# Performance work log

Hardware: AMD Instinct MI355X
Metric: run time of the kernel (lower is better)

The kernel has to match this reference:

```python
import jax, jax.numpy as jnp
import numpy as np

B, L, S, H, E = 2, 2048, 2048, 16, 64


def setup_inputs() -> dict:
    key = jax.random.key(0)
    kq, kk, kv = jax.random.split(key, 3)
    queries = jax.random.normal(kq, (B, L, H, E), dtype=jnp.float32)
    keys = jax.random.normal(kk, (B, S, H, E), dtype=jnp.float32)
    values = jax.random.normal(kv, (B, S, H, E), dtype=jnp.float32)
    attn_mask = jnp.ones((B, 1, L, S), dtype=jnp.float32)  # >0.5 means attend
    return {"queries": queries, "keys": keys, "values": values, "attn_mask": attn_mask}


def reference(queries, keys, values, attn_mask):
    # queries: [B,L,H,E], keys/values: [B,S,H,E], attn_mask broadcastable to [B,H,L,S]
    E_ = queries.shape[-1]
    scale = 1.0 / np.sqrt(E_).astype(np.float32)
    scores = jnp.einsum('blhe,bshe->bhls', queries, keys)  # [B,H,L,S]
    large_negative = jnp.float32(-1e9)
    scores = scores + jnp.where(attn_mask > 0.5, jnp.float32(0.0), large_negative)
    A = jax.nn.softmax(scale * scores, axis=-1)  # dropout p=0.0 -> identity
    V = jnp.einsum('bhls,bshd->bhld', A, values)  # [B,H,L,D]
    return V
```

## Files before the change

### kernel.cpp

```cpp
#include <hip/hip_runtime.h>

typedef float    f32x4 __attribute__((ext_vector_type(4)));
typedef _Float16 f16x2 __attribute__((ext_vector_type(2)));
typedef _Float16 f16x4 __attribute__((ext_vector_type(4)));
typedef _Float16 f16x8 __attribute__((ext_vector_type(8)));
typedef int      i32x4 __attribute__((ext_vector_type(4)));

namespace {
constexpr int B_ = 2, L_ = 2048, S_ = 2048, H_ = 16, E_ = 64;
constexpr int MBLK = 128;
constexpr int NT = 64;
constexpr int NTILES = S_ / NT;

#define SCALE2f 0.1803368801111204f
#define MBIAS2f -1.8033688e8f

constexpr size_t KHOFF = (size_t)1 << 20;
constexpr size_t VHOFF = KHOFF + (size_t)B_ * H_ * S_ * E_ * 2;

__device__ __forceinline__ f16x2 cvt2(float a, float b) {
  return __builtin_bit_cast(f16x2, __builtin_amdgcn_cvt_pkrtz(a, b));
}
__device__ __forceinline__ int pkh(float a, float b) {
  return __builtin_bit_cast(int, __builtin_amdgcn_cvt_pkrtz(a, b));
}
union H8 { f16x8 v; i32x4 i; };
union H4 { f16x4 v; f16x2 h[2]; };

#define GLOAD_LDS16(g, l)                                              \
  __builtin_amdgcn_global_load_lds(                                    \
      (const __attribute__((address_space(1))) void*)(g),              \
      (__attribute__((address_space(3))) void*)(l), 16, 0, 0)
}

extern "C" __global__ __launch_bounds__(256)
void maskpack_kernel(const float* __restrict__ Mg, unsigned long long* __restrict__ Wb) {
  const int w    = (int)((blockIdx.x * 256 + threadIdx.x) >> 6);
  const int lane = threadIdx.x & 63;
  const float* src = Mg + (size_t)w * 2048 + lane;
  unsigned long long* dst = Wb + (size_t)w * 32;
#pragma unroll 8
  for (int j = 0; j < 32; ++j) {
    const unsigned long long bits = __ballot(src[j * 64] > 0.5f);
    if (lane == 0) dst[j] = bits;
  }
}

extern "C" __global__ __launch_bounds__(256)
void kcvt_kernel(const float* __restrict__ Kg, _Float16* __restrict__ Kh) {
  const int idx = blockIdx.x * 256 + threadIdx.x;
  const int j = idx & 7;
  const int h = (idx >> 3) & (H_ - 1);
  const int s = (idx >> 7) & (S_ - 1);
  const int b = idx >> 18;
  const float* src = Kg + ((((size_t)b * S_ + s) * H_ + h) << 6) + j * 8;
  f32x4 x = *(const f32x4*)src, y = *(const f32x4*)(src + 4);
  i32x4 w = {pkh(x[0], x[1]), pkh(x[2], x[3]), pkh(y[0], y[1]), pkh(y[2], y[3])};
  *(i32x4*)(Kh + ((((size_t)b * H_ + h) * S_ + s) << 6) + j * 8) = w;
}

extern "C" __global__ __launch_bounds__(256)
void vcvt_kernel(const float* __restrict__ Vg, _Float16* __restrict__ Vh) {
  __shared__ _Float16 T[64][72];
  const int bid = blockIdx.x;
  const int st = bid & 31;
  const int h  = (bid >> 5) & (H_ - 1);
  const int b  = bid >> 9;
  const int t  = threadIdx.x;
  const int sl = t >> 2;
  const int e0 = (t & 3) << 4;
  const float* src = Vg + ((((size_t)b * S_ + st * 64 + sl) * H_ + h) << 6) + e0;
#pragma unroll
  for (int i = 0; i < 4; ++i) {
    f32x4 x = *(const f32x4*)(src + i * 4);
#pragma unroll
    for (int c = 0; c < 4; ++c) T[e0 + i * 4 + c][sl] = (_Float16)x[c];
  }
  __syncthreads();
  const int er = t >> 2;
  const int s0 = (t & 3) << 4;
  _Float16* dst = Vh + (((((size_t)b * H_ + h) << 6) + er) * S_) + st * 64 + s0;
  *(i32x4*)dst       = *(const i32x4*)&T[er][s0];
  *(i32x4*)(dst + 8) = *(const i32x4*)&T[er][s0 + 8];
}

extern "C" __global__ __launch_bounds__(256, 2)
void fattn_kernel(const float* __restrict__ Qg, const _Float16* __restrict__ Kh,
                  const _Float16* __restrict__ Vh, const unsigned long long* __restrict__ Wb,
                  float* __restrict__ Og) {
  __shared__ __align__(16) _Float16 Ks[2][NT][64];
  __shared__ __align__(16) _Float16 Vt[2][E_][64];

  const int tid  = threadIdx.x;
  const int wv   = tid >> 6;
  const int lane = tid & 63;
  const int qd   = lane >> 4;
  const int cl   = lane & 15;
  const int sw   = cl & 7;

  const int bid = blockIdx.x;
  const int qb  = bid >> 5;
  const int bh  = bid & 31;
  const int h   = bh & (H_ - 1);
  const int b   = bh >> 4;

  const int l0 = qb * MBLK + wv * 32;

  f16x8 qf[2][2];
#pragma unroll
  for (int mt = 0; mt < 2; ++mt) {
    const float* qp = Qg + ((((size_t)b * L_ + (l0 + mt * 16 + cl)) * H_ + h) << 6);
#pragma unroll
    for (int kb = 0; kb < 2; ++kb) {
      const int e0 = qd * 8 + kb * 32;
      f32x4 x = *(const f32x4*)(qp + e0);
      f32x4 y = *(const f32x4*)(qp + e0 + 4);
      H8 u;
      u.i = (i32x4){pkh(x[0], x[1]), pkh(x[2], x[3]), pkh(y[0], y[1]), pkh(y[2], y[3])};
      qf[mt][kb] = u.v;
    }
  }

  const int rl  = lane >> 3;
  const int gsl = lane & 7;
  const int gsw = gsl ^ rl;
  const _Float16* khb = Kh + ((((size_t)b * H_ + h) * S_) << 6);
  const _Float16* vhb = Vh + ((((size_t)b * H_ + h) << 6) * (size_t)S_);

  const unsigned long long* wbp = Wb + (((size_t)b * L_ + (l0 + cl)) << 5);

  auto dma = [&](int buf, int t) {
#pragma unroll
    for (int p = 0; p < 2; ++p) {
      const int r0 = p * 32 + wv * 8;
      const _Float16* ksrc = khb + (((size_t)(t * 64 + r0 + rl)) << 6) + gsw * 8;
      GLOAD_LDS16(ksrc, &Ks[buf][r0][0]);
      const _Float16* vsrc = vhb + (size_t)(r0 + rl) * S_ + t * 64 + gsw * 8;
      GLOAD_LDS16(vsrc, &Vt[buf][r0][0]);
    }
  };

  const f32x4 zero4 = {0.f, 0.f, 0.f, 0.f};
  f32x4 acc[2][4];
#pragma unroll
  for (int mt = 0; mt < 2; ++mt)
#pragma unroll
    for (int et = 0; et < 4; ++et) acc[mt][et] = zero4;
  f32x4 rs4[2] = {zero4, zero4};

  dma(0, 0);
  unsigned long long mwcur = wbp[0];

  for (int t = 0; t < NTILES; ++t) {
    const int cb = t & 1;
    __syncthreads();

    if (t + 1 < NTILES) dma(cb ^ 1, t + 1);
    unsigned long long mwnext = 0;
    if (t + 1 < NTILES) mwnext = wbp[t + 1];

    f32x4 sc[4][2];
#pragma unroll
    for (int nt = 0; nt < 4; ++nt) {
      const _Float16* krow = &Ks[cb][nt * 16 + cl][0];
      const f16x8 a0 = *(const f16x8*)(krow + ((qd ^ sw) << 3));
      const f16x8 a1 = *(const f16x8*)(krow + (((qd + 4) ^ sw) << 3));
#pragma unroll
      for (int mt = 0; mt < 2; ++mt) {
        f32x4 c = zero4;
        c = __builtin_amdgcn_mfma_f32_16x16x32_f16(a0, qf[mt][0], c, 0, 0, 0);
        c = __builtin_amdgcn_mfma_f32_16x16x32_f16(a1, qf[mt][1], c, 0, 0, 0);
        sc[nt][mt] = c;
      }
    }

    f16x4 pa[2][4];
    if (mwcur == ~0ull) {
#pragma unroll
      for (int mt = 0; mt < 2; ++mt)
#pragma unroll
        for (int nt = 0; nt < 4; ++nt) {
          f32x4 p;
#pragma unroll
          for (int r = 0; r < 4; ++r)
            p[r] = __builtin_amdgcn_exp2f(sc[nt][mt][r] * SCALE2f);
          rs4[mt] += p;
          H4 u;
          u.h[0] = cvt2(p[0], p[1]);
          u.h[1] = cvt2(p[2], p[3]);
          pa[mt][nt] = u.v;
        }
    } else {
      const unsigned lo = (unsigned)mwcur;
      const unsigned hi = (unsigned)(mwcur >> 32);
#pragma unroll
      for (int mt = 0; mt < 2; ++mt)
#pragma unroll
        for (int nt = 0; nt < 4; ++nt) {
          const unsigned shm = ((nt < 2) ? lo : hi) >> ((nt & 1) * 16 + qd * 4);
          f32x4 p;
#pragma unroll
          for (int r = 0; r < 4; ++r) {
            const float bias = (shm & (1u << r)) ? 0.f : MBIAS2f;
            p[r] = __builtin_amdgcn_exp2f(__builtin_fmaf(sc[nt][mt][r], SCALE2f, bias));
          }
          rs4[mt] += p;
          H4 u;
          u.h[0] = cvt2(p[0], p[1]);
          u.h[1] = cvt2(p[2], p[3]);
          pa[mt][nt] = u.v;
        }
    }

#pragma unroll
    for (int nt = 0; nt < 4; ++nt)
#pragma unroll
      for (int et = 0; et < 4; ++et) {
        const _Float16* vrow = &Vt[cb][et * 16 + cl][0];
        const f16x4 bv = *(const f16x4*)(vrow + ((((2 * nt + (qd >> 1)) ^ sw) << 3) + ((qd & 1) << 2)));
        acc[0][et] = __builtin_amdgcn_mfma_f32_16x16x16f16(pa[0][nt], bv, acc[0][et], 0, 0, 0);
        acc[1][et] = __builtin_amdgcn_mfma_f32_16x16x16f16(pa[1][nt], bv, acc[1][et], 0, 0, 0);
      }

    mwcur = mwnext;
  }

#pragma unroll
  for (int mt = 0; mt < 2; ++mt) {
    float v = rs4[mt][0] + rs4[mt][1] + rs4[mt][2] + rs4[mt][3];
    v += __shfl_xor(v, 16, 64);
    v += __shfl_xor(v, 32, 64);
#pragma unroll
    for (int r = 0; r < 4; ++r) {
      const float invq = 1.0f / __shfl(v, qd * 4 + r, 64);
      const int l = l0 + mt * 16 + qd * 4 + r;
      float* op = Og + ((((size_t)b * H_ + h) * L_ + l) << 6) + cl;
#pragma unroll
      for (int et = 0; et < 4; ++et) op[et * 16] = acc[mt][et][r] * invq;
    }
  }
}

extern "C" void kernel_launch(void* const* d_in, const int* in_sizes, int n_in,
                              void* d_out, int out_size, void* d_ws, size_t ws_size,
                              hipStream_t stream) {
  const float* Q = (const float*)d_in[0];
  const float* K = (const float*)d_in[1];
  const float* V = (const float*)d_in[2];
  const float* M = (const float*)d_in[3];
  float* O = (float*)d_out;
  unsigned long long* Wb = (unsigned long long*)d_ws;
  _Float16* Khp = (_Float16*)((char*)d_ws + KHOFF);
  _Float16* Vhp = (_Float16*)((char*)d_ws + VHOFF);

  hipLaunchKernelGGL(maskpack_kernel, dim3(B_ * L_ / 4), dim3(256), 0, stream, M, Wb);
  hipLaunchKernelGGL(kcvt_kernel, dim3(B_ * S_ * H_ * 8 / 256), dim3(256), 0, stream, K, Khp);
  hipLaunchKernelGGL(vcvt_kernel, dim3(B_ * H_ * (S_ / 64)), dim3(256), 0, stream, V, Vhp);
  hipLaunchKernelGGL(fattn_kernel, dim3(B_ * H_ * (L_ / MBLK)), dim3(256), 0, stream,
                     Q, Khp, Vhp, Wb, O);
}
```

Measured before the change: 177.1 us.

## Use 8 waves of 16 query rows per block and vectorize mask packing

The attention kernel now runs 512 threads per block, with each wave owning 16 query rows instead of 32. Register pressure per wave drops and more waves are resident to hide latency, but each K/V tile in LDS is reused by fewer rows per wave. The mask packer now has each thread read 16 contiguous floats with vector loads and write a 16-bit word, replacing per-wave ballots with strided scalar loads.

New measurement: 166.6 us. -5.9%, faster.

```diff
diff --git a/kernel.cpp b/kernel.cpp
--- a/kernel.cpp
+++ b/kernel.cpp
@@ -35,15 +35,16 @@
 
 extern "C" __global__ __launch_bounds__(256)
 void maskpack_kernel(const float* __restrict__ Mg, unsigned long long* __restrict__ Wb) {
-  const int w    = (int)((blockIdx.x * 256 + threadIdx.x) >> 6);
-  const int lane = threadIdx.x & 63;
-  const float* src = Mg + (size_t)w * 2048 + lane;
-  unsigned long long* dst = Wb + (size_t)w * 32;
-#pragma unroll 8
-  for (int j = 0; j < 32; ++j) {
-    const unsigned long long bits = __ballot(src[j * 64] > 0.5f);
-    if (lane == 0) dst[j] = bits;
-  }
+  const int u = blockIdx.x * 256 + threadIdx.x;
+  const float* src = Mg + (size_t)u * 16;
+  unsigned m = 0;
+#pragma unroll
+  for (int i = 0; i < 4; ++i) {
+    f32x4 x = *(const f32x4*)(src + i * 4);
+#pragma unroll
+    for (int c = 0; c < 4; ++c) m |= (x[c] > 0.5f ? 1u : 0u) << (i * 4 + c);
+  }
+  ((unsigned short*)Wb)[u] = (unsigned short)m;
 }
 
 extern "C" __global__ __launch_bounds__(256)
@@ -84,7 +85,7 @@
   *(i32x4*)(dst + 8) = *(const i32x4*)&T[er][s0 + 8];
 }
 
-extern "C" __global__ __launch_bounds__(256, 2)
+extern "C" __global__ __launch_bounds__(512, 4)
 void fattn_kernel(const float* __restrict__ Qg, const _Float16* __restrict__ Kh,
                   const _Float16* __restrict__ Vh, const unsigned long long* __restrict__ Wb,
                   float* __restrict__ Og) {
@@ -104,12 +105,11 @@
   const int h   = bh & (H_ - 1);
   const int b   = bh >> 4;
 
-  const int l0 = qb * MBLK + wv * 32;
-
-  f16x8 qf[2][2];
-#pragma unroll
-  for (int mt = 0; mt < 2; ++mt) {
-    const float* qp = Qg + ((((size_t)b * L_ + (l0 + mt * 16 + cl)) * H_ + h) << 6);
+  const int l0 = qb * MBLK + wv * 16;
+
+  f16x8 qf[2];
+  {
+    const float* qp = Qg + ((((size_t)b * L_ + (l0 + cl)) * H_ + h) << 6);
 #pragma unroll
     for (int kb = 0; kb < 2; ++kb) {
       const int e0 = qd * 8 + kb * 32;
@@ -117,7 +117,7 @@
       f32x4 y = *(const f32x4*)(qp + e0 + 4);
       H8 u;
       u.i = (i32x4){pkh(x[0], x[1]), pkh(x[2], x[3]), pkh(y[0], y[1]), pkh(y[2], y[3])};
-      qf[mt][kb] = u.v;
+      qf[kb] = u.v;
     }
   }
 
@@ -130,23 +130,18 @@
   const unsigned long long* wbp = Wb + (((size_t)b * L_ + (l0 + cl)) << 5);
 
   auto dma = [&](int buf, int t) {
-#pragma unroll
-    for (int p = 0; p < 2; ++p) {
-      const int r0 = p * 32 + wv * 8;
-      const _Float16* ksrc = khb + (((size_t)(t * 64 + r0 + rl)) << 6) + gsw * 8;
-      GLOAD_LDS16(ksrc, &Ks[buf][r0][0]);
-      const _Float16* vsrc = vhb + (size_t)(r0 + rl) * S_ + t * 64 + gsw * 8;
-      GLOAD_LDS16(vsrc, &Vt[buf][r0][0]);
-    }
+    const int r0 = wv * 8;
+    const _Float16* ksrc = khb + (((size_t)(t * 64 + r0 + rl)) << 6) + gsw * 8;
+    GLOAD_LDS16(ksrc, &Ks[buf][r0][0]);
+    const _Float16* vsrc = vhb + (size_t)(r0 + rl) * S_ + t * 64 + gsw * 8;
+    GLOAD_LDS16(vsrc, &Vt[buf][r0][0]);
   };
 
   const f32x4 zero4 = {0.f, 0.f, 0.f, 0.f};
-  f32x4 acc[2][4];
-#pragma unroll
-  for (int mt = 0; mt < 2; ++mt)
-#pragma unroll
-    for (int et = 0; et < 4; ++et) acc[mt][et] = zero4;
-  f32x4 rs4[2] = {zero4, zero4};
+  f32x4 acc[4];
+#pragma unroll
+  for (int et = 0; et < 4; ++et) acc[et] = zero4;
+  f32x4 rs4 = zero4;
 
   dma(0, 0);
   unsigned long long mwcur = wbp[0];
@@ -159,57 +154,50 @@
     unsigned long long mwnext = 0;
     if (t + 1 < NTILES) mwnext = wbp[t + 1];
 
-    f32x4 sc[4][2];
+    f32x4 sc[4];
 #pragma unroll
     for (int nt = 0; nt < 4; ++nt) {
       const _Float16* krow = &Ks[cb][nt * 16 + cl][0];
       const f16x8 a0 = *(const f16x8*)(krow + ((qd ^ sw) << 3));
       const f16x8 a1 = *(const f16x8*)(krow + (((qd + 4) ^ sw) << 3));
-#pragma unroll
-      for (int mt = 0; mt < 2; ++mt) {
-        f32x4 c = zero4;
-        c = __builtin_amdgcn_mfma_f32_16x16x32_f16(a0, qf[mt][0], c, 0, 0, 0);
-        c = __builtin_amdgcn_mfma_f32_16x16x32_f16(a1, qf[mt][1], c, 0, 0, 0);
-        sc[nt][mt] = c;
+      f32x4 c = zero4;
+      c = __builtin_amdgcn_mfma_f32_16x16x32_f16(a0, qf[0], c, 0, 0, 0);
+      c = __builtin_amdgcn_mfma_f32_16x16x32_f16(a1, qf[1], c, 0, 0, 0);
+      sc[nt] = c;
+    }
+
+    f16x4 pa[4];
+    if (mwcur == ~0ull) {
+#pragma unroll
+      for (int nt = 0; nt < 4; ++nt) {
+        f32x4 p;
+#pragma unroll
+        for (int r = 0; r < 4; ++r)
+          p[r] = __builtin_amdgcn_exp2f(sc[nt][r] * SCALE2f);
+        rs4 += p;
+        H4 u;
+        u.h[0] = cvt2(p[0], p[1]);
+        u.h[1] = cvt2(p[2], p[3]);
+        pa[nt] = u.v;
       }
-    }
-
-    f16x4 pa[2][4];
-    if (mwcur == ~0ull) {
-#pragma unroll
-      for (int mt = 0; mt < 2; ++mt)
-#pragma unroll
-        for (int nt = 0; nt < 4; ++nt) {
-          f32x4 p;
-#pragma unroll
-          for (int r = 0; r < 4; ++r)
-            p[r] = __builtin_amdgcn_exp2f(sc[nt][mt][r] * SCALE2f);
-          rs4[mt] += p;
-          H4 u;
-          u.h[0] = cvt2(p[0], p[1]);
-          u.h[1] = cvt2(p[2], p[3]);
-          pa[mt][nt] = u.v;
-        }
     } else {
       const unsigned lo = (unsigned)mwcur;
       const unsigned hi = (unsigned)(mwcur >> 32);
 #pragma unroll
-      for (int mt = 0; mt < 2; ++mt)
-#pragma unroll
-        for (int nt = 0; nt < 4; ++nt) {
-          const unsigned shm = ((nt < 2) ? lo : hi) >> ((nt & 1) * 16 + qd * 4);
-          f32x4 p;
-#pragma unroll
-          for (int r = 0; r < 4; ++r) {
-            const float bias = (shm & (1u << r)) ? 0.f : MBIAS2f;
-            p[r] = __builtin_amdgcn_exp2f(__builtin_fmaf(sc[nt][mt][r], SCALE2f, bias));
-          }
-          rs4[mt] += p;
-          H4 u;
-          u.h[0] = cvt2(p[0], p[1]);
-          u.h[1] = cvt2(p[2], p[3]);
-          pa[mt][nt] = u.v;
+      for (int nt = 0; nt < 4; ++nt) {
+        const unsigned shm = ((nt < 2) ? lo : hi) >> ((nt & 1) * 16 + qd * 4);
+        f32x4 p;
+#pragma unroll
+        for (int r = 0; r < 4; ++r) {
+          const float bias = (shm & (1u << r)) ? 0.f : MBIAS2f;
+          p[r] = __builtin_amdgcn_exp2f(__builtin_fmaf(sc[nt][r], SCALE2f, bias));
         }
+        rs4 += p;
+        H4 u;
+        u.h[0] = cvt2(p[0], p[1]);
+        u.h[1] = cvt2(p[2], p[3]);
+        pa[nt] = u.v;
+      }
     }
 
 #pragma unroll
@@ -218,25 +206,23 @@
       for (int et = 0; et < 4; ++et) {
         const _Float16* vrow = &Vt[cb][et * 16 + cl][0];
         const f16x4 bv = *(const f16x4*)(vrow + ((((2 * nt + (qd >> 1)) ^ sw) << 3) + ((qd & 1) << 2)));
-        acc[0][et] = __builtin_amdgcn_mfma_f32_16x16x16f16(pa[0][nt], bv, acc[0][et], 0, 0, 0);
-        acc[1][et] = __builtin_amdgcn_mfma_f32_16x16x16f16(pa[1][nt], bv, acc[1][et], 0, 0, 0);
+        acc[et] = __builtin_amdgcn_mfma_f32_16x16x16f16(pa[nt], bv, acc[et], 0, 0, 0);
       }
 
     mwcur = mwnext;
   }
 
-#pragma unroll
-  for (int mt = 0; mt < 2; ++mt) {
-    float v = rs4[mt][0] + rs4[mt][1] + rs4[mt][2] + rs4[mt][3];
+  {
+    float v = rs4[0] + rs4[1] + rs4[2] + rs4[3];
     v += __shfl_xor(v, 16, 64);
     v += __shfl_xor(v, 32, 64);
 #pragma unroll
     for (int r = 0; r < 4; ++r) {
       const float invq = 1.0f / __shfl(v, qd * 4 + r, 64);
-      const int l = l0 + mt * 16 + qd * 4 + r;
+      const int l = l0 + qd * 4 + r;
       float* op = Og + ((((size_t)b * H_ + h) * L_ + l) << 6) + cl;
 #pragma unroll
-      for (int et = 0; et < 4; ++et) op[et * 16] = acc[mt][et][r] * invq;
+      for (int et = 0; et < 4; ++et) op[et * 16] = acc[et][r] * invq;
     }
   }
 }
@@ -253,9 +239,9 @@
   _Float16* Khp = (_Float16*)((char*)d_ws + KHOFF);
   _Float16* Vhp = (_Float16*)((char*)d_ws + VHOFF);
 
-  hipLaunchKernelGGL(maskpack_kernel, dim3(B_ * L_ / 4), dim3(256), 0, stream, M, Wb);
+  hipLaunchKernelGGL(maskpack_kernel, dim3(B_ * L_ * S_ / (16 * 256)), dim3(256), 0, stream, M, Wb);
   hipLaunchKernelGGL(kcvt_kernel, dim3(B_ * S_ * H_ * 8 / 256), dim3(256), 0, stream, K, Khp);
   hipLaunchKernelGGL(vcvt_kernel, dim3(B_ * H_ * (S_ / 64)), dim3(256), 0, stream, V, Vhp);
-  hipLaunchKernelGGL(fattn_kernel, dim3(B_ * H_ * (L_ / MBLK)), dim3(256), 0, stream,
+  hipLaunchKernelGGL(fattn_kernel, dim3(B_ * H_ * (L_ / MBLK)), dim3(512), 0, stream,
                      Q, Khp, Vhp, Wb, O);
 }
```

## Split key range across two wave groups and fuse prep kernels into one launch

Applied to the files above, without the earlier changes.

The attention kernel now runs 512 threads per block: two groups of four waves each process half of the key tiles for the same 128 query rows. At the end, partial accumulators and row sums are exchanged through shared memory before normalisation. This raises parallelism per block (more waves in flight across 512 blocks) at the cost of a final cross-group reduction and more LDS use. The mask-pack, K-convert and V-transpose kernels are merged into one launch, with the mask packing rewritten to be per-thread, which removes two launch overheads.

New measurement: 234.5 us. +32.4%, slower.

```diff
diff --git a/kernel.cpp b/kernel.cpp
--- a/kernel.cpp
+++ b/kernel.cpp
@@ -10,7 +10,7 @@
 constexpr int B_ = 2, L_ = 2048, S_ = 2048, H_ = 16, E_ = 64;
 constexpr int MBLK = 128;
 constexpr int NT = 64;
-constexpr int NTILES = S_ / NT;
+constexpr int NTILES_G = 16;
 
 #define SCALE2f 0.1803368801111204f
 #define MBIAS2f -1.8033688e8f
@@ -34,66 +34,68 @@
 }
 
 extern "C" __global__ __launch_bounds__(256)
-void maskpack_kernel(const float* __restrict__ Mg, unsigned long long* __restrict__ Wb) {
-  const int w    = (int)((blockIdx.x * 256 + threadIdx.x) >> 6);
-  const int lane = threadIdx.x & 63;
-  const float* src = Mg + (size_t)w * 2048 + lane;
-  unsigned long long* dst = Wb + (size_t)w * 32;
-#pragma unroll 8
-  for (int j = 0; j < 32; ++j) {
-    const unsigned long long bits = __ballot(src[j * 64] > 0.5f);
-    if (lane == 0) dst[j] = bits;
-  }
-}
-
-extern "C" __global__ __launch_bounds__(256)
-void kcvt_kernel(const float* __restrict__ Kg, _Float16* __restrict__ Kh) {
-  const int idx = blockIdx.x * 256 + threadIdx.x;
-  const int j = idx & 7;
-  const int h = (idx >> 3) & (H_ - 1);
-  const int s = (idx >> 7) & (S_ - 1);
-  const int b = idx >> 18;
-  const float* src = Kg + ((((size_t)b * S_ + s) * H_ + h) << 6) + j * 8;
-  f32x4 x = *(const f32x4*)src, y = *(const f32x4*)(src + 4);
-  i32x4 w = {pkh(x[0], x[1]), pkh(x[2], x[3]), pkh(y[0], y[1]), pkh(y[2], y[3])};
-  *(i32x4*)(Kh + ((((size_t)b * H_ + h) * S_ + s) << 6) + j * 8) = w;
-}
-
-extern "C" __global__ __launch_bounds__(256)
-void vcvt_kernel(const float* __restrict__ Vg, _Float16* __restrict__ Vh) {
+void prep_kernel(const float* __restrict__ Kg, const float* __restrict__ Vg,
+                 const float* __restrict__ Mg, _Float16* __restrict__ Kh,
+                 _Float16* __restrict__ Vh, unsigned long long* __restrict__ Wb) {
   __shared__ _Float16 T[64][72];
   const int bid = blockIdx.x;
-  const int st = bid & 31;
-  const int h  = (bid >> 5) & (H_ - 1);
-  const int b  = bid >> 9;
-  const int t  = threadIdx.x;
-  const int sl = t >> 2;
-  const int e0 = (t & 3) << 4;
-  const float* src = Vg + ((((size_t)b * S_ + st * 64 + sl) * H_ + h) << 6) + e0;
-#pragma unroll
-  for (int i = 0; i < 4; ++i) {
-    f32x4 x = *(const f32x4*)(src + i * 4);
-#pragma unroll
-    for (int c = 0; c < 4; ++c) T[e0 + i * 4 + c][sl] = (_Float16)x[c];
-  }
-  __syncthreads();
-  const int er = t >> 2;
-  const int s0 = (t & 3) << 4;
-  _Float16* dst = Vh + (((((size_t)b * H_ + h) << 6) + er) * S_) + st * 64 + s0;
-  *(i32x4*)dst       = *(const i32x4*)&T[er][s0];
-  *(i32x4*)(dst + 8) = *(const i32x4*)&T[er][s0 + 8];
-}
-
-extern "C" __global__ __launch_bounds__(256, 2)
+  const int t   = threadIdx.x;
+
+  if (bid < 2048) {
+    const int idx = bid * 256 + t;
+    const int j = idx & 7;
+    const int h = (idx >> 3) & (H_ - 1);
+    const int s = (idx >> 7) & (S_ - 1);
+    const int b = idx >> 18;
+    const float* src = Kg + ((((size_t)b * S_ + s) * H_ + h) << 6) + j * 8;
+    f32x4 x = *(const f32x4*)src, y = *(const f32x4*)(src + 4);
+    i32x4 w = {pkh(x[0], x[1]), pkh(x[2], x[3]), pkh(y[0], y[1]), pkh(y[2], y[3])};
+    *(i32x4*)(Kh + ((((size_t)b * H_ + h) * S_ + s) << 6) + j * 8) = w;
+  } else if (bid < 4096) {
+    const int u = (bid - 2048) * 256 + t;
+    const float* src = Mg + (size_t)u * 16;
+    unsigned m = 0;
+#pragma unroll
+    for (int i = 0; i < 4; ++i) {
+      f32x4 x = *(const f32x4*)(src + i * 4);
+#pragma unroll
+      for (int c = 0; c < 4; ++c) m |= (x[c] > 0.5f ? 1u : 0u) << (i * 4 + c);
+    }
+    ((unsigned short*)Wb)[u] = (unsigned short)m;
+  } else {
+    const int vb = bid - 4096;
+    const int st = vb & 31;
+    const int h  = (vb >> 5) & (H_ - 1);
+    const int b  = vb >> 9;
+    const int sl = t >> 2;
+    const int e0 = (t & 3) << 4;
+    const float* src = Vg + ((((size_t)b * S_ + st * 64 + sl) * H_ + h) << 6) + e0;
+#pragma unroll
+    for (int i = 0; i < 4; ++i) {
+      f32x4 x = *(const f32x4*)(src + i * 4);
+#pragma unroll
+      for (int c = 0; c < 4; ++c) T[e0 + i * 4 + c][sl] = (_Float16)x[c];
+    }
+    __syncthreads();
+    const int er = t >> 2;
+    const int s0 = (t & 3) << 4;
+    _Float16* dst = Vh + (((((size_t)b * H_ + h) << 6) + er) * S_) + st * 64 + s0;
+    *(i32x4*)dst       = *(const i32x4*)&T[er][s0];
+    *(i32x4*)(dst + 8) = *(const i32x4*)&T[er][s0 + 8];
+  }
+}
+
+extern "C" __global__ __launch_bounds__(512, 4)
 void fattn_kernel(const float* __restrict__ Qg, const _Float16* __restrict__ Kh,
                   const _Float16* __restrict__ Vh, const unsigned long long* __restrict__ Wb,
                   float* __restrict__ Og) {
-  __shared__ __align__(16) _Float16 Ks[2][NT][64];
-  __shared__ __align__(16) _Float16 Vt[2][E_][64];
+  __shared__ __align__(16) _Float16 smem[2][2][2][64][64];
 
   const int tid  = threadIdx.x;
   const int wv   = tid >> 6;
   const int lane = tid & 63;
+  const int g    = wv >> 2;
+  const int wq   = wv & 3;
   const int qd   = lane >> 4;
   const int cl   = lane & 15;
   const int sw   = cl & 7;
@@ -104,7 +106,7 @@
   const int h   = bh & (H_ - 1);
   const int b   = bh >> 4;
 
-  const int l0 = qb * MBLK + wv * 32;
+  const int l0 = qb * MBLK + wq * 32;
 
   f16x8 qf[2][2];
 #pragma unroll
@@ -127,16 +129,17 @@
   const _Float16* khb = Kh + ((((size_t)b * H_ + h) * S_) << 6);
   const _Float16* vhb = Vh + ((((size_t)b * H_ + h) << 6) * (size_t)S_);
 
-  const unsigned long long* wbp = Wb + (((size_t)b * L_ + (l0 + cl)) << 5);
+  const unsigned long long* wbp = Wb + (((size_t)b * L_ + (l0 + cl)) << 5) + g * NTILES_G;
 
   auto dma = [&](int buf, int t) {
+    const int ts = g * NTILES_G + t;
 #pragma unroll
     for (int p = 0; p < 2; ++p) {
-      const int r0 = p * 32 + wv * 8;
-      const _Float16* ksrc = khb + (((size_t)(t * 64 + r0 + rl)) << 6) + gsw * 8;
-      GLOAD_LDS16(ksrc, &Ks[buf][r0][0]);
-      const _Float16* vsrc = vhb + (size_t)(r0 + rl) * S_ + t * 64 + gsw * 8;
-      GLOAD_LDS16(vsrc, &Vt[buf][r0][0]);
+      const int r0 = p * 32 + wq * 8;
+      const _Float16* ksrc = khb + (((size_t)(ts * 64 + r0 + rl)) << 6) + gsw * 8;
+      GLOAD_LDS16(ksrc, &smem[g][0][buf][r0][0]);
+      const _Float16* vsrc = vhb + (size_t)(r0 + rl) * S_ + ts * 64 + gsw * 8;
+      GLOAD_LDS16(vsrc, &smem[g][1][buf][r0][0]);
     }
   };
 
@@ -151,18 +154,18 @@
   dma(0, 0);
   unsigned long long mwcur = wbp[0];
 
-  for (int t = 0; t < NTILES; ++t) {
+  for (int t = 0; t < NTILES_G; ++t) {
     const int cb = t & 1;
     __syncthreads();
 
-    if (t + 1 < NTILES) dma(cb ^ 1, t + 1);
+    if (t + 1 < NTILES_G) dma(cb ^ 1, t + 1);
     unsigned long long mwnext = 0;
-    if (t + 1 < NTILES) mwnext = wbp[t + 1];
+    if (t + 1 < NTILES_G) mwnext = wbp[t + 1];
 
     f32x4 sc[4][2];
 #pragma unroll
     for (int nt = 0; nt < 4; ++nt) {
-      const _Float16* krow = &Ks[cb][nt * 16 + cl][0];
+      const _Float16* krow = &smem[g][0][cb][nt * 16 + cl][0];
       const f16x8 a0 = *(const f16x8*)(krow + ((qd ^ sw) << 3));
       const f16x8 a1 = *(const f16x8*)(krow + (((qd + 4) ^ sw) << 3));
 #pragma unroll
@@ -216,7 +219,7 @@
     for (int nt = 0; nt < 4; ++nt)
 #pragma unroll
       for (int et = 0; et < 4; ++et) {
-        const _Float16* vrow = &Vt[cb][et * 16 + cl][0];
+        const _Float16* vrow = &smem[g][1][cb][et * 16 + cl][0];
         const f16x4 bv = *(const f16x4*)(vrow + ((((2 * nt + (qd >> 1)) ^ sw) << 3) + ((qd & 1) << 2)));
         acc[0][et] = __builtin_amdgcn_mfma_f32_16x16x16f16(pa[0][nt], bv, acc[0][et], 0, 0, 0);
         acc[1][et] = __builtin_amdgcn_mfma_f32_16x16x16f16(pa[1][nt], bv, acc[1][et], 0, 0, 0);
@@ -225,18 +228,33 @@
     mwcur = mwnext;
   }
 
+  __syncthreads();
+  f32x4* xb = (f32x4*)smem;
+  f32x4* rb = xb + 2 * 4 * 2 * 2 * 64;
+  const int gd = 1 - g;
 #pragma unroll
   for (int mt = 0; mt < 2; ++mt) {
-    float v = rs4[mt][0] + rs4[mt][1] + rs4[mt][2] + rs4[mt][3];
+#pragma unroll
+    for (int ei = 0; ei < 2; ++ei)
+      xb[((((gd * 4 + wq) * 2 + mt) * 2 + ei) << 6) + lane] = acc[mt][2 * gd + ei];
+    rb[(((g * 4 + wq) * 2 + mt) << 6) + lane] = rs4[mt];
+  }
+  __syncthreads();
+#pragma unroll
+  for (int mt = 0; mt < 2; ++mt) {
+    const f32x4 rsum = rs4[mt] + rb[(((gd * 4 + wq) * 2 + mt) << 6) + lane];
+    float v = rsum[0] + rsum[1] + rsum[2] + rsum[3];
     v += __shfl_xor(v, 16, 64);
     v += __shfl_xor(v, 32, 64);
+    const f32x4 a0 = acc[mt][2 * g + 0] + xb[((((g * 4 + wq) * 2 + mt) * 2 + 0) << 6) + lane];
+    const f32x4 a1 = acc[mt][2 * g + 1] + xb[((((g * 4 + wq) * 2 + mt) * 2 + 1) << 6) + lane];
 #pragma unroll
     for (int r = 0; r < 4; ++r) {
       const float invq = 1.0f / __shfl(v, qd * 4 + r, 64);
       const int l = l0 + mt * 16 + qd * 4 + r;
       float* op = Og + ((((size_t)b * H_ + h) * L_ + l) << 6) + cl;
-#pragma unroll
-      for (int et = 0; et < 4; ++et) op[et * 16] = acc[mt][et][r] * invq;
+      op[(2 * g + 0) * 16] = a0[r] * invq;
+      op[(2 * g + 1) * 16] = a1[r] * invq;
     }
   }
 }
@@ -253,9 +271,7 @@
   _Float16* Khp = (_Float16*)((char*)d_ws + KHOFF);
   _Float16* Vhp = (_Float16*)((char*)d_ws + VHOFF);
 
-  hipLaunchKernelGGL(maskpack_kernel, dim3(B_ * L_ / 4), dim3(256), 0, stream, M, Wb);
-  hipLaunchKernelGGL(kcvt_kernel, dim3(B_ * S_ * H_ * 8 / 256), dim3(256), 0, stream, K, Khp);
-  hipLaunchKernelGGL(vcvt_kernel, dim3(B_ * H_ * (S_ / 64)), dim3(256), 0, stream, V, Vhp);
-  hipLaunchKernelGGL(fattn_kernel, dim3(B_ * H_ * (L_ / MBLK)), dim3(256), 0, stream,
+  hipLaunchKernelGGL(prep_kernel, dim3(5120), dim3(256), 0, stream, K, V, M, Khp, Vhp, Wb);
+  hipLaunchKernelGGL(fattn_kernel, dim3(B_ * H_ * (L_ / MBLK)), dim3(512), 0, stream,
                      Q, Khp, Vhp, Wb, O);
 }
```
